# Optimization experiments

Measured on AMD Instinct MI355X. Metric: run time of the kernel, lower is better.

## Reference

```python
import jax, jax.numpy as jnp
import numpy as np

CTX = (16, 16)          # rel_pos_ctx_size
N_HEADS = 12
HEAD_DIM = 64           # emb_dim // n_heads


def _make_rel_pos_ids(ctx):
    # Faithful replication of the torch buffer construction.
    rge = [2 * s - 1 for s in ctx]
    coords = np.stack(np.meshgrid(*[np.arange(s) for s in ctx], indexing='ij'))  # [2, *ctx]
    coords = coords.reshape(len(ctx), -1)                                        # [2, n]
    rel = coords[:, :, None] - coords[:, None, :]                                # [2, n, n]
    rel = rel.reshape(len(ctx), -1)                                              # [2, n*n]
    rel = rel + (np.array(ctx)[:, None] - 1)
    ids = np.ravel_multi_index(tuple(rel), tuple(rge))                           # [n*n]
    return jnp.asarray(ids, dtype=jnp.int32)


def setup_inputs() -> dict:
    key = jax.random.key(0)
    ks = jax.random.split(key, 6)
    b, n, e = 128, 256, 768
    std_in = 1.0 / np.sqrt(e)
    return {
        'x': jax.random.normal(ks[0], (b, n, e), jnp.float32),
        'W_qkv': jax.random.normal(ks[1], (e, 3 * e), jnp.float32) * std_in,
        'b_qkv': jax.random.normal(ks[2], (3 * e,), jnp.float32) * 0.02,
        'W_out': jax.random.normal(ks[3], (e, e), jnp.float32) * std_in,
        'b_out': jax.random.normal(ks[4], (e,), jnp.float32) * 0.02,
        'rel_bias_table': jax.random.normal(ks[5], ((2 * CTX[0] - 1) * (2 * CTX[1] - 1), N_HEADS), jnp.float32) * 0.02,
        'rel_pos_ids': _make_rel_pos_ids(CTX),
    }


def reference(x, W_qkv, b_qkv, W_out, b_out, rel_bias_table, rel_pos_ids):
    b, n, e = x.shape
    h, d = N_HEADS, HEAD_DIM
    scale = d ** -0.5
    # fused qkv projection: 'b n (k h d) -> k b h n d'
    qkv = (x @ W_qkv + b_qkv).reshape(b, n, 3, h, d)
    q, k, v = (jnp.transpose(qkv, (2, 0, 3, 1, 4))[i] for i in range(3))  # each [b h n d]
    # gathered relative-position bias: [n*n, h] -> [h, n, n]
    bias = rel_bias_table[rel_pos_ids].reshape(n, n, h).transpose(2, 0, 1)
    scores = jnp.einsum('bhnd,bhmd->bhnm', q, k) * scale + bias
    attn = jax.nn.softmax(scores, axis=-1)
    out = jnp.einsum('bhnm,bhmd->bhnd', attn, v)
    out = out.transpose(0, 2, 1, 3).reshape(b, n, e)  # 'b h n d -> b n (h d)'
    return out @ W_out + b_out
```

## Files before the change

### kernel.cpp

```cpp
#include <hip/hip_runtime.h>
#include <cstdint>
#include <cstddef>

typedef __bf16 bf16x8 __attribute__((ext_vector_type(8)));
typedef __bf16 bf16x4 __attribute__((ext_vector_type(4)));
typedef float f32x4 __attribute__((ext_vector_type(4)));
static_assert(sizeof(bf16x8) == 16, "bf16x8 must be 16B");
static_assert(sizeof(bf16x4) == 8, "bf16x4 must be 8B");
static_assert(sizeof(f32x4) == 16, "f32x4 must be 16B");

#define MFMA16(a, b, c) __builtin_amdgcn_mfma_f32_16x16x32_bf16((a), (b), (c), 0, 0, 0)

__device__ __forceinline__ void gload_lds16(const void* g, void* l) {
  __builtin_amdgcn_global_load_lds(
      (const __attribute__((address_space(1))) void*)g,
      (__attribute__((address_space(3))) void*)l, 16, 0, 0);
}

__global__ __launch_bounds__(256) void conv_x_kernel(const float* __restrict__ in,
                                                     __bf16* __restrict__ out) {
  size_t i = ((size_t)blockIdx.x * 256 + threadIdx.x) * 4;
  const float4 v = *(const float4*)(in + i);
  out[i + 0] = (__bf16)v.x;
  out[i + 1] = (__bf16)v.y;
  out[i + 2] = (__bf16)v.z;
  out[i + 3] = (__bf16)v.w;
}

__global__ __launch_bounds__(256) void transpose_conv_kernel(const float* __restrict__ in,
                                                             __bf16* __restrict__ out,
                                                             int K, int N) {
  __shared__ float tile[32][33];
  const int n0 = blockIdx.x * 32, k0 = blockIdx.y * 32;
  const int tx = threadIdx.x, ty = threadIdx.y;
#pragma unroll
  for (int i = 0; i < 4; ++i)
    tile[ty * 4 + i][tx] = in[(size_t)(k0 + ty * 4 + i) * N + n0 + tx];
  __syncthreads();
#pragma unroll
  for (int i = 0; i < 4; ++i)
    out[(size_t)(n0 + ty * 4 + i) * K + k0 + tx] = (__bf16)tile[tx][ty * 4 + i];
}

__global__ __launch_bounds__(256) void bias_gather_kernel(const float* __restrict__ table,
                                                          const int* __restrict__ ids,
                                                          float* __restrict__ biasT) {
  const int idx = blockIdx.x * 256 + threadIdx.x;
  const int h = idx >> 16, ji = idx & 65535;
  const int j = ji >> 8, i = ji & 255;
  biasT[idx] = table[ids[i * 256 + j] * 12 + h];
}

template <int MODE, int NT>
__global__ __launch_bounds__(256) void gemm_kernel(const __bf16* __restrict__ A,
                                                   const __bf16* __restrict__ Bt,
                                                   const float* __restrict__ bias,
                                                   void* __restrict__ out0,
                                                   __bf16* __restrict__ kbuf,
                                                   const int M, const int N, const int K) {
  constexpr bool TRANS = (MODE != 2);
  __shared__ __bf16 smem[2 * 128 * 64];
  const int tid = threadIdx.x;
  const int lane = tid & 63, w = tid >> 6;
  const int m16 = lane & 15, q4 = lane >> 4;
  const int wm = w & 1, wn = w >> 1;
  const int id = blockIdx.x;
  const int mi = id & 7;
  const int rest = id >> 3;
  const int ny = rest % NT;
  const int g = rest / NT;
  const int m0 = (g * 8 + mi) * 128;
  const int n0 = ny * 128;

  const __bf16* ag[4];
  const __bf16* bg[4];
  __bf16* la[4];
  __bf16* lb[4];
#pragma unroll
  for (int i = 0; i < 4; ++i) {
    const int row = w * 32 + i * 8 + (lane >> 3);
    const int col = ((lane & 7) ^ (row & 7)) * 8;
    ag[i] = A + (size_t)(m0 + row) * K + col;
    bg[i] = Bt + (size_t)(n0 + row) * K + col;
    la[i] = &smem[(w * 32 + i * 8) * 64];
    lb[i] = &smem[8192 + (w * 32 + i * 8) * 64];
  }

  int aoff[4][2], boff[4][2];
#pragma unroll
  for (int t = 0; t < 4; ++t)
#pragma unroll
    for (int kh = 0; kh < 2; ++kh) {
      const int ra = wm * 64 + t * 16 + m16;
      aoff[t][kh] = ra * 64 + (((kh * 4 + q4) ^ (ra & 7)) * 8);
      const int rb = wn * 64 + t * 16 + m16;
      boff[t][kh] = 8192 + rb * 64 + (((kh * 4 + q4) ^ (rb & 7)) * 8);
    }

  f32x4 acc[4][4] = {};
  const int ksteps = K >> 6;
  for (int kt = 0; kt < ksteps; ++kt) {
#pragma unroll
    for (int i = 0; i < 4; ++i) gload_lds16(ag[i], la[i]);
#pragma unroll
    for (int i = 0; i < 4; ++i) gload_lds16(bg[i], lb[i]);
#pragma unroll
    for (int i = 0; i < 4; ++i) { ag[i] += 64; bg[i] += 64; }
    __syncthreads();
    bf16x8 af[4][2], bfr[4][2];
#pragma unroll
    for (int t = 0; t < 4; ++t)
#pragma unroll
      for (int kh = 0; kh < 2; ++kh) {
        af[t][kh] = *(const bf16x8*)&smem[aoff[t][kh]];
        bfr[t][kh] = *(const bf16x8*)&smem[boff[t][kh]];
      }
#pragma unroll
    for (int kh = 0; kh < 2; ++kh)
#pragma unroll
      for (int i = 0; i < 4; ++i)
#pragma unroll
        for (int j = 0; j < 4; ++j) {
          if (TRANS)
            acc[i][j] = MFMA16(bfr[i][kh], af[j][kh], acc[i][j]);
          else
            acc[i][j] = MFMA16(af[i][kh], bfr[j][kh], acc[i][j]);
        }
    __syncthreads();
  }

  const int gnb = n0 + wn * 64;
  const int gmb = m0 + wm * 64;

  if (MODE == 0) {
    __bf16* qb = (__bf16*)out0;
    const int which = (n0 >= 768);
    __bf16* dst = which ? kbuf : qb;
    const float qscale = which ? 1.0f : 0.125f;
    const int bi = gmb >> 8;
    const int tokb = gmb & 255;
#pragma unroll
    for (int i = 0; i < 4; ++i) {
      const int gn0 = gnb + i * 16 + q4 * 4;
      const f32x4 bn = *(const f32x4*)&bias[gn0];
      const int rem0 = gn0 - which * 768;
      const int hh = rem0 >> 6, dd0 = rem0 & 63;
      __bf16* base = dst + ((size_t)bi * 12 + hh) * 16384 + dd0;
#pragma unroll
      for (int j = 0; j < 4; ++j) {
        const int tok = tokb + j * 16 + m16;
        bf16x4 pk;
#pragma unroll
        for (int r = 0; r < 4; ++r) pk[r] = (__bf16)((acc[i][j][r] + bn[r]) * qscale);
        *(bf16x4*)(base + (size_t)tok * 64) = pk;
      }
    }
  } else if (MODE == 2) {
    __bf16* vt = (__bf16*)out0;
    const int bi = gmb >> 8;
    const int tokb = gmb & 255;
#pragma unroll
    for (int j = 0; j < 4; ++j) {
      const int gn = gnb + j * 16 + m16;
      const float bn = bias[gn];
      const int hh = gn >> 6, dd = gn & 63;
      __bf16* base = vt + (((size_t)bi * 12 + hh) * 64 + dd) * 256;
#pragma unroll
      for (int i = 0; i < 4; ++i) {
        const int tok0 = tokb + i * 16 + q4 * 4;
        bf16x4 pk;
#pragma unroll
        for (int r = 0; r < 4; ++r) pk[r] = (__bf16)(acc[i][j][r] + bn);
        *(bf16x4*)(base + tok0) = pk;
      }
    }
  } else {
    float* out = (float*)out0;
#pragma unroll
    for (int i = 0; i < 4; ++i) {
      const int gn0 = gnb + i * 16 + q4 * 4;
      const f32x4 bn = *(const f32x4*)&bias[gn0];
#pragma unroll
      for (int j = 0; j < 4; ++j) {
        const int gm = gmb + j * 16 + m16;
        f32x4 v;
#pragma unroll
        for (int r = 0; r < 4; ++r) v[r] = acc[i][j][r] + bn[r];
        *(f32x4*)(out + (size_t)gm * N + gn0) = v;
      }
    }
  }
}

__global__ __launch_bounds__(512, 4) void attn_kernel(const __bf16* __restrict__ qb,
                                                      const __bf16* __restrict__ kb,
                                                      const __bf16* __restrict__ vtb,
                                                      const float* __restrict__ biasT,
                                                      __bf16* __restrict__ o_ws) {
  __shared__ __bf16 klds[256 * 64];
  __shared__ __bf16 vlds[64 * 256];
  const int tid = threadIdx.x;
  const int lane = tid & 63, w = tid >> 6;
  const int m16 = lane & 15, q4 = lane >> 4;
  const int b = blockIdx.x, h = blockIdx.y;
  const size_t bh = (size_t)b * 12 + h;
  const __bf16* Q = qb + bh * (256 * 64);
  const __bf16* Kp = kb + bh * (256 * 64);
  const __bf16* Vt = vtb + bh * (64 * 256);
  const float* BhT = biasT + (size_t)h * 65536;
  const int qbase = blockIdx.z * 128;
  const int qrow0 = qbase + w * 16;

#pragma unroll
  for (int i = 0; i < 4; ++i) {
    const int row = w * 32 + i * 8 + (lane >> 3);
    const int col = ((lane & 7) ^ (row & 7)) * 8;
    gload_lds16(Kp + (size_t)row * 64 + col, &klds[(w * 32 + i * 8) * 64]);
  }
#pragma unroll
  for (int i = 0; i < 4; ++i) {
    const int row = w * 8 + i * 2 + (lane >> 5);
    const int g = lane & 31;
    const int gp = (g & 24) | ((g & 7) ^ (row & 7));
    gload_lds16(Vt + (size_t)row * 256 + gp * 8, &vlds[(w * 8 + i * 2) * 256]);
  }

  bf16x8 qf[2];
#pragma unroll
  for (int t = 0; t < 2; ++t)
    qf[t] = *(const bf16x8*)(Q + (size_t)(qrow0 + m16) * 64 + t * 32 + q4 * 8);

  __syncthreads();

  f32x4 s[16];
#pragma unroll
  for (int c = 0; c < 16; ++c) {
    const int krow = c * 16 + m16;
    const bf16x8 kf0 = *(const bf16x8*)&klds[krow * 64 + ((q4 ^ (m16 & 7)) * 8)];
    const bf16x8 kf1 = *(const bf16x8*)&klds[krow * 64 + (((4 + q4) ^ (m16 & 7)) * 8)];
    f32x4 z = {0.f, 0.f, 0.f, 0.f};
    z = MFMA16(qf[0], kf0, z);
    s[c] = MFMA16(qf[1], kf1, z);
  }

#pragma unroll
  for (int c = 0; c < 16; ++c) {
    const f32x4 bv = *(const f32x4*)&BhT[(size_t)(c * 16 + m16) * 256 + qrow0 + q4 * 4];
    s[c] += bv;
  }

  float linv[4];
#pragma unroll
  for (int r = 0; r < 4; ++r) {
    float mx = s[0][r];
#pragma unroll
    for (int c = 1; c < 16; ++c) mx = fmaxf(mx, s[c][r]);
    mx = fmaxf(mx, __shfl_xor(mx, 1));
    mx = fmaxf(mx, __shfl_xor(mx, 2));
    mx = fmaxf(mx, __shfl_xor(mx, 4));
    mx = fmaxf(mx, __shfl_xor(mx, 8));
    float sum = 0.f;
#pragma unroll
    for (int c = 0; c < 16; ++c) {
      const float p = exp2f((s[c][r] - mx) * 1.4426950408889634f);
      s[c][r] = p;
      sum += p;
    }
    sum += __shfl_xor(sum, 1);
    sum += __shfl_xor(sum, 2);
    sum += __shfl_xor(sum, 4);
    sum += __shfl_xor(sum, 8);
    linv[r] = 1.f / sum;
  }

  __syncthreads();

  f32x4 o[4] = {};
  __bf16* P = &klds[w * 1152];
#pragma unroll
  for (int ch = 0; ch < 4; ++ch) {
#pragma unroll
    for (int cc = 0; cc < 4; ++cc)
#pragma unroll
      for (int r = 0; r < 4; ++r)
        P[(q4 * 4 + r) * 72 + cc * 16 + m16] = (__bf16)s[ch * 4 + cc][r];
#pragma unroll
    for (int kt = 0; kt < 2; ++kt) {
      const bf16x8 pf = *(const bf16x8*)(P + m16 * 72 + kt * 32 + q4 * 8);
#pragma unroll
      for (int dt = 0; dt < 4; ++dt) {
        const int vrow = dt * 16 + m16;
        const bf16x8 vf = *(const bf16x8*)&vlds[vrow * 256 + ch * 64 +
                                                (((kt * 4 + q4) ^ (m16 & 7)) * 8)];
        o[dt] = MFMA16(pf, vf, o[dt]);
      }
    }
  }

#pragma unroll
  for (int dt = 0; dt < 4; ++dt)
#pragma unroll
    for (int r = 0; r < 4; ++r) {
      const float v = o[dt][r] * linv[r];
      const size_t row = (size_t)b * 256 + qrow0 + q4 * 4 + r;
      o_ws[row * 768 + h * 64 + dt * 16 + m16] = (__bf16)v;
    }
}

extern "C" void kernel_launch(void* const* d_in, const int* in_sizes, int n_in,
                              void* d_out, int out_size, void* d_ws, size_t ws_size,
                              hipStream_t stream) {
  const float* x = (const float*)d_in[0];
  const float* Wqkv = (const float*)d_in[1];
  const float* bqkv = (const float*)d_in[2];
  const float* Wout = (const float*)d_in[3];
  const float* bout = (const float*)d_in[4];
  const float* table = (const float*)d_in[5];
  const int* ids = (const int*)d_in[6];
  float* out = (float*)d_out;

  char* ws = (char*)d_ws;
  __bf16* xbf = (__bf16*)ws;
  __bf16* wqkvt = (__bf16*)(ws + 50331648);
  __bf16* woutt = (__bf16*)(ws + 53870592);
  __bf16* qbuf = (__bf16*)(ws + 55050240);
  __bf16* kbuf = (__bf16*)(ws + 105381888);
  __bf16* vtbuf = (__bf16*)(ws + 155713536);
  float* biasT = (float*)(ws + 206045184);

  conv_x_kernel<<<24576, 256, 0, stream>>>(x, xbf);
  transpose_conv_kernel<<<dim3(72, 24), dim3(32, 8), 0, stream>>>(Wqkv, wqkvt, 768, 2304);
  transpose_conv_kernel<<<dim3(24, 24), dim3(32, 8), 0, stream>>>(Wout, woutt, 768, 768);
  bias_gather_kernel<<<3072, 256, 0, stream>>>(table, ids, biasT);
  gemm_kernel<0, 12><<<3072, 256, 0, stream>>>(xbf, wqkvt, bqkv, qbuf, kbuf,
                                               32768, 2304, 768);
  gemm_kernel<2, 6><<<1536, 256, 0, stream>>>(xbf, wqkvt + (size_t)1536 * 768,
                                              bqkv + 1536, vtbuf, nullptr,
                                              32768, 768, 768);
  attn_kernel<<<dim3(128, 12, 2), 512, 0, stream>>>(qbuf, kbuf, vtbuf, biasT, xbf );
  gemm_kernel<1, 6><<<1536, 256, 0, stream>>>(xbf, woutt, bout, out, nullptr,
                                              32768, 768, 768);
}
```

Measured before the change: 505.0 us.

## Replace GEMM with 256x256-tile 8-wave double-buffered pipelined kernel

Replaces the 128x128, 4-wave, single-buffer GEMM with a 256x256 tile kernel using 8 waves and double-buffered LDS (128KB). Global-to-LDS loads for the next k-step are issued in quarters between MFMA phases, with manual vmcnt/lgkmcnt waits, barriers and setprio to overlap memory with compute. The workgroup index is remapped in chunks of 8 for L2 locality. This raises per-block data reuse and hides load latency, but cuts the block count to a few hundred, which may leave CUs underfilled and adds fragile hand-tuned synchronization.

```diff
diff --git a/kernel.cpp b/kernel.cpp
--- a/kernel.cpp
+++ b/kernel.cpp
@@ -10,6 +10,9 @@
 static_assert(sizeof(f32x4) == 16, "f32x4 must be 16B");
 
 #define MFMA16(a, b, c) __builtin_amdgcn_mfma_f32_16x16x32_bf16((a), (b), (c), 0, 0, 0)
+#define SBAR() __builtin_amdgcn_s_barrier()
+#define LGKM0() asm volatile("s_waitcnt lgkmcnt(0)" ::: "memory")
+#define VMCNT(n_) asm volatile("s_waitcnt vmcnt(" #n_ ")" ::: "memory")
 
 __device__ __forceinline__ void gload_lds16(const void* g, void* l) {
   __builtin_amdgcn_global_load_lds(
@@ -52,107 +55,171 @@
 }
 
 template <int MODE, int NT>
-__global__ __launch_bounds__(256) void gemm_kernel(const __bf16* __restrict__ A,
-                                                   const __bf16* __restrict__ Bt,
-                                                   const float* __restrict__ bias,
-                                                   void* __restrict__ out0,
-                                                   __bf16* __restrict__ kbuf,
-                                                   const int M, const int N, const int K) {
+__global__ __launch_bounds__(512, 2) void gemm8_kernel(const __bf16* __restrict__ A,
+                                                       const __bf16* __restrict__ Bt,
+                                                       const float* __restrict__ bias,
+                                                       void* __restrict__ out0,
+                                                       __bf16* __restrict__ kbuf,
+                                                       const int M, const int N, const int K) {
   constexpr bool TRANS = (MODE != 2);
-  __shared__ __bf16 smem[2 * 128 * 64];
+  __shared__ __align__(16) __bf16 smem[65536];
   const int tid = threadIdx.x;
   const int lane = tid & 63, w = tid >> 6;
   const int m16 = lane & 15, q4 = lane >> 4;
   const int wm = w & 1, wn = w >> 1;
+
+  const int nwg = NT * (M >> 8);
+  const int chunk = nwg >> 3;
   const int id = blockIdx.x;
-  const int mi = id & 7;
-  const int rest = id >> 3;
-  const int ny = rest % NT;
-  const int g = rest / NT;
-  const int m0 = (g * 8 + mi) * 128;
-  const int n0 = ny * 128;
-
-  const __bf16* ag[4];
-  const __bf16* bg[4];
-  __bf16* la[4];
-  __bf16* lb[4];
-#pragma unroll
-  for (int i = 0; i < 4; ++i) {
-    const int row = w * 32 + i * 8 + (lane >> 3);
-    const int col = ((lane & 7) ^ (row & 7)) * 8;
-    ag[i] = A + (size_t)(m0 + row) * K + col;
-    bg[i] = Bt + (size_t)(n0 + row) * K + col;
-    la[i] = &smem[(w * 32 + i * 8) * 64];
-    lb[i] = &smem[8192 + (w * 32 + i * 8) * 64];
-  }
-
-  int aoff[4][2], boff[4][2];
-#pragma unroll
-  for (int t = 0; t < 4; ++t)
-#pragma unroll
-    for (int kh = 0; kh < 2; ++kh) {
-      const int ra = wm * 64 + t * 16 + m16;
-      aoff[t][kh] = ra * 64 + (((kh * 4 + q4) ^ (ra & 7)) * 8);
-      const int rb = wn * 64 + t * 16 + m16;
-      boff[t][kh] = 8192 + rb * 64 + (((kh * 4 + q4) ^ (rb & 7)) * 8);
-    }
-
-  f32x4 acc[4][4] = {};
-  const int ksteps = K >> 6;
-  for (int kt = 0; kt < ksteps; ++kt) {
-#pragma unroll
-    for (int i = 0; i < 4; ++i) gload_lds16(ag[i], la[i]);
-#pragma unroll
-    for (int i = 0; i < 4; ++i) gload_lds16(bg[i], lb[i]);
-#pragma unroll
-    for (int i = 0; i < 4; ++i) { ag[i] += 64; bg[i] += 64; }
-    __syncthreads();
-    bf16x8 af[4][2], bfr[4][2];
-#pragma unroll
-    for (int t = 0; t < 4; ++t)
-#pragma unroll
-      for (int kh = 0; kh < 2; ++kh) {
-        af[t][kh] = *(const bf16x8*)&smem[aoff[t][kh]];
-        bfr[t][kh] = *(const bf16x8*)&smem[boff[t][kh]];
-      }
+  const int wg = (id & 7) * chunk + (id >> 3);
+  const int mi = wg / NT, ni = wg - mi * NT;
+  const int m0 = mi << 8, n0 = ni << 8;
+
+  const int srow = w * 8 + (lane >> 3);
+  const int sg = ((lane & 7) ^ (srow & 7)) * 8;
+  const __bf16* ag = A + (size_t)(m0 + srow) * K + sg;
+  const __bf16* bg = Bt + (size_t)(n0 + srow) * K + sg;
+  const int dstw = w * 512;
+
+  const int g0 = (q4 ^ (m16 & 7)) * 8;
+  const int g1 = ((4 + q4) ^ (m16 & 7)) * 8;
+  const int abase = (wm * 128 + m16) * 64;
+  const int bbase = 16384 + (wn * 64 + m16) * 64;
+
+  const int nt = K >> 6;
+
+#define STAGE(T_, mat_, h_)                                                        \
+  do {                                                                             \
+    const __bf16* s_ = ((mat_) ? bg : ag) + (size_t)(T_)*64 + (size_t)(h_)*128 * K; \
+    __bf16* d_ = &smem[((T_)&1) * 32768 + (mat_)*16384 + (h_)*8192 + dstw];        \
+    gload_lds16(s_, d_);                                                           \
+    gload_lds16(s_ + (size_t)64 * K, d_ + 4096);                                   \
+  } while (0)
+
+#define MM(a_, b_, c_) (TRANS ? MFMA16((b_), (a_), (c_)) : MFMA16((a_), (b_), (c_)))
+
+  STAGE(0, 0, 0);
+  STAGE(0, 0, 1);
+  STAGE(0, 1, 0);
+  STAGE(0, 1, 1);
+  STAGE(1, 0, 0);
+  VMCNT(2);
+  SBAR();
+
+  f32x4 acc[8][4] = {};
+  for (int T = 0; T < nt; ++T) {
+    const int base = (T & 1) * 32768;
+    bf16x8 a[4][2], b0[2][2], b1[2][2];
+
+#pragma unroll
+    for (int fm = 0; fm < 4; ++fm) {
+      a[fm][0] = *(const bf16x8*)&smem[base + abase + fm * 1024 + g0];
+      a[fm][1] = *(const bf16x8*)&smem[base + abase + fm * 1024 + g1];
+    }
+#pragma unroll
+    for (int fn = 0; fn < 2; ++fn) {
+      b0[fn][0] = *(const bf16x8*)&smem[base + bbase + fn * 1024 + g0];
+      b0[fn][1] = *(const bf16x8*)&smem[base + bbase + fn * 1024 + g1];
+    }
+    if (T + 1 < nt) STAGE(T + 1, 0, 1);
+    SBAR();
+    LGKM0();
+    __builtin_amdgcn_s_setprio(1);
 #pragma unroll
     for (int kh = 0; kh < 2; ++kh)
 #pragma unroll
-      for (int i = 0; i < 4; ++i)
-#pragma unroll
-        for (int j = 0; j < 4; ++j) {
-          if (TRANS)
-            acc[i][j] = MFMA16(bfr[i][kh], af[j][kh], acc[i][j]);
-          else
-            acc[i][j] = MFMA16(af[i][kh], bfr[j][kh], acc[i][j]);
-        }
-    __syncthreads();
-  }
-
+      for (int fm = 0; fm < 4; ++fm)
+#pragma unroll
+        for (int fn = 0; fn < 2; ++fn)
+          acc[fm][fn] = MM(a[fm][kh], b0[fn][kh], acc[fm][fn]);
+    __builtin_amdgcn_s_setprio(0);
+    SBAR();
+
+#pragma unroll
+    for (int fn = 0; fn < 2; ++fn) {
+      b1[fn][0] = *(const bf16x8*)&smem[base + bbase + 2048 + fn * 1024 + g0];
+      b1[fn][1] = *(const bf16x8*)&smem[base + bbase + 2048 + fn * 1024 + g1];
+    }
+    if (T + 1 < nt) {
+      STAGE(T + 1, 1, 0);
+      STAGE(T + 1, 1, 1);
+    }
+    SBAR();
+    LGKM0();
+    __builtin_amdgcn_s_setprio(1);
+#pragma unroll
+    for (int kh = 0; kh < 2; ++kh)
+#pragma unroll
+      for (int fm = 0; fm < 4; ++fm)
+#pragma unroll
+        for (int fn = 0; fn < 2; ++fn)
+          acc[fm][2 + fn] = MM(a[fm][kh], b1[fn][kh], acc[fm][2 + fn]);
+    __builtin_amdgcn_s_setprio(0);
+    SBAR();
+
+#pragma unroll
+    for (int fm = 0; fm < 4; ++fm) {
+      a[fm][0] = *(const bf16x8*)&smem[base + abase + 4096 + fm * 1024 + g0];
+      a[fm][1] = *(const bf16x8*)&smem[base + abase + 4096 + fm * 1024 + g1];
+    }
+    SBAR();
+    LGKM0();
+    __builtin_amdgcn_s_setprio(1);
+#pragma unroll
+    for (int kh = 0; kh < 2; ++kh)
+#pragma unroll
+      for (int fm = 0; fm < 4; ++fm)
+#pragma unroll
+        for (int fn = 0; fn < 2; ++fn)
+          acc[4 + fm][2 + fn] = MM(a[fm][kh], b1[fn][kh], acc[4 + fm][2 + fn]);
+    __builtin_amdgcn_s_setprio(0);
+    SBAR();
+
+    if (T + 2 < nt) {
+      STAGE(T + 2, 0, 0);
+      VMCNT(2);
+    } else if (T + 1 < nt) {
+      VMCNT(0);
+    }
+    SBAR();
+    __builtin_amdgcn_s_setprio(1);
+#pragma unroll
+    for (int kh = 0; kh < 2; ++kh)
+#pragma unroll
+      for (int fm = 0; fm < 4; ++fm)
+#pragma unroll
+        for (int fn = 0; fn < 2; ++fn)
+          acc[4 + fm][fn] = MM(a[fm][kh], b0[fn][kh], acc[4 + fm][fn]);
+    __builtin_amdgcn_s_setprio(0);
+    SBAR();
+  }
+#undef STAGE
+#undef MM
+
+  const int gmb = m0 + wm * 128;
   const int gnb = n0 + wn * 64;
-  const int gmb = m0 + wm * 64;
 
   if (MODE == 0) {
     __bf16* qb = (__bf16*)out0;
-    const int which = (n0 >= 768);
+    const int which = (gnb >= 768);
     __bf16* dst = which ? kbuf : qb;
     const float qscale = which ? 1.0f : 0.125f;
     const int bi = gmb >> 8;
     const int tokb = gmb & 255;
 #pragma unroll
-    for (int i = 0; i < 4; ++i) {
-      const int gn0 = gnb + i * 16 + q4 * 4;
+    for (int fn = 0; fn < 4; ++fn) {
+      const int gn0 = gnb + fn * 16 + q4 * 4;
       const f32x4 bn = *(const f32x4*)&bias[gn0];
       const int rem0 = gn0 - which * 768;
       const int hh = rem0 >> 6, dd0 = rem0 & 63;
-      __bf16* base = dst + ((size_t)bi * 12 + hh) * 16384 + dd0;
-#pragma unroll
-      for (int j = 0; j < 4; ++j) {
-        const int tok = tokb + j * 16 + m16;
+      __bf16* basep = dst + ((size_t)bi * 12 + hh) * 16384 + dd0;
+#pragma unroll
+      for (int fm = 0; fm < 8; ++fm) {
+        const int tok = tokb + fm * 16 + m16;
         bf16x4 pk;
 #pragma unroll
-        for (int r = 0; r < 4; ++r) pk[r] = (__bf16)((acc[i][j][r] + bn[r]) * qscale);
-        *(bf16x4*)(base + (size_t)tok * 64) = pk;
+        for (int r = 0; r < 4; ++r) pk[r] = (__bf16)((acc[fm][fn][r] + bn[r]) * qscale);
+        *(bf16x4*)(basep + (size_t)tok * 64) = pk;
       }
     }
   } else if (MODE == 2) {
@@ -160,32 +227,32 @@
     const int bi = gmb >> 8;
     const int tokb = gmb & 255;
 #pragma unroll
-    for (int j = 0; j < 4; ++j) {
-      const int gn = gnb + j * 16 + m16;
+    for (int fn = 0; fn < 4; ++fn) {
+      const int gn = gnb + fn * 16 + m16;
       const float bn = bias[gn];
       const int hh = gn >> 6, dd = gn & 63;
-      __bf16* base = vt + (((size_t)bi * 12 + hh) * 64 + dd) * 256;
-#pragma unroll
-      for (int i = 0; i < 4; ++i) {
-        const int tok0 = tokb + i * 16 + q4 * 4;
+      __bf16* basep = vt + (((size_t)bi * 12 + hh) * 64 + dd) * 256;
+#pragma unroll
+      for (int fm = 0; fm < 8; ++fm) {
+        const int tok0 = tokb + fm * 16 + q4 * 4;
         bf16x4 pk;
 #pragma unroll
-        for (int r = 0; r < 4; ++r) pk[r] = (__bf16)(acc[i][j][r] + bn);
-        *(bf16x4*)(base + tok0) = pk;
+        for (int r = 0; r < 4; ++r) pk[r] = (__bf16)(acc[fm][fn][r] + bn);
+        *(bf16x4*)(basep + tok0) = pk;
       }
     }
   } else {
     float* out = (float*)out0;
 #pragma unroll
-    for (int i = 0; i < 4; ++i) {
-      const int gn0 = gnb + i * 16 + q4 * 4;
+    for (int fn = 0; fn < 4; ++fn) {
+      const int gn0 = gnb + fn * 16 + q4 * 4;
       const f32x4 bn = *(const f32x4*)&bias[gn0];
 #pragma unroll
-      for (int j = 0; j < 4; ++j) {
-        const int gm = gmb + j * 16 + m16;
+      for (int fm = 0; fm < 8; ++fm) {
+        const int gm = gmb + fm * 16 + m16;
         f32x4 v;
 #pragma unroll
-        for (int r = 0; r < 4; ++r) v[r] = acc[i][j][r] + bn[r];
+        for (int r = 0; r < 4; ++r) v[r] = acc[fm][fn][r] + bn[r];
         *(f32x4*)(out + (size_t)gm * N + gn0) = v;
       }
     }
@@ -332,12 +399,12 @@
   transpose_conv_kernel<<<dim3(72, 24), dim3(32, 8), 0, stream>>>(Wqkv, wqkvt, 768, 2304);
   transpose_conv_kernel<<<dim3(24, 24), dim3(32, 8), 0, stream>>>(Wout, woutt, 768, 768);
   bias_gather_kernel<<<3072, 256, 0, stream>>>(table, ids, biasT);
-  gemm_kernel<0, 12><<<3072, 256, 0, stream>>>(xbf, wqkvt, bqkv, qbuf, kbuf,
-                                               32768, 2304, 768);
-  gemm_kernel<2, 6><<<1536, 256, 0, stream>>>(xbf, wqkvt + (size_t)1536 * 768,
+  gemm8_kernel<0, 6><<<768, 512, 0, stream>>>(xbf, wqkvt, bqkv, qbuf, kbuf,
+                                              32768, 1536, 768);
+  gemm8_kernel<2, 3><<<384, 512, 0, stream>>>(xbf, wqkvt + (size_t)1536 * 768,
                                               bqkv + 1536, vtbuf, nullptr,
                                               32768, 768, 768);
   attn_kernel<<<dim3(128, 12, 2), 512, 0, stream>>>(qbuf, kbuf, vtbuf, biasT, xbf );
-  gemm_kernel<1, 6><<<1536, 256, 0, stream>>>(xbf, woutt, bout, out, nullptr,
+  gemm8_kernel<1, 3><<<384, 512, 0, stream>>>(xbf, woutt, bout, out, nullptr,
                                               32768, 768, 768);
 }
```

After: 502.4 us. No clear change (-0.5%).
